# Optimization experiments

Measured on AMD Instinct MI355X. Metric: run time of the kernel, lower is better.

Reference implementation:

```python
import jax, jax.numpy as jnp
import numpy as np

B, C, H, W = 1, 256, 96, 96
C8 = C // 8
N = H * W


def setup_inputs() -> dict:
    key = jax.random.key(0)
    ks = jax.random.split(key, 12)
    inp = {
        "x": jax.random.normal(ks[0], (B, C, H, W), jnp.float32),
        "x_encoder": jax.random.normal(ks[1], (B, C, H, W), jnp.float32),
        # 1x1 conv params (weight stored as [out, in] matrices)
        "q_w": jax.random.normal(ks[2], (C8, C), jnp.float32) * 0.05,
        "q_b": jax.random.normal(ks[3], (C8,), jnp.float32) * 0.05,
        "k_w": jax.random.normal(ks[4], (C8, C), jnp.float32) * 0.05,
        "k_b": jax.random.normal(ks[5], (C8,), jnp.float32) * 0.05,
        "v_w": jax.random.normal(ks[6], (C, C), jnp.float32) * 0.05,
        "v_b": jax.random.normal(ks[7], (C,), jnp.float32) * 0.05,
        # positional bias parameters
        "h_pos": jax.random.normal(ks[8], (1, C8, H, 1), jnp.float32),
        "w_pos": jax.random.normal(ks[9], (1, C8, 1, W), jnp.float32),
        # gamma is zero-init in the module; use a random scalar for a non-trivial test
        "gamma": jax.random.normal(ks[10], (1,), jnp.float32),
    }
    return inp


def reference(x, x_encoder, q_w, q_b, k_w, k_b, v_w, v_b, h_pos, w_pos, gamma):
    b, c, h, w = x.shape
    n = h * w
    c8 = q_w.shape[0]
    # 1x1 convs == per-pixel linear maps
    query = (jnp.einsum('bchw,oc->bohw', x, q_w) + q_b[None, :, None, None])
    query = query.reshape(b, c8, n).transpose(0, 2, 1)            # [B, N, C8]
    key = (jnp.einsum('bchw,oc->bohw', x_encoder, k_w) + k_b[None, :, None, None])
    key = key.reshape(b, c8, n)                                   # [B, C8, N]
    # positional bias: broadcast-add then flatten, same as (height+width).view
    pos = (h_pos + w_pos).reshape(1, c8, n)                       # [1, C8, N]
    # energy = Q K^T + Q pos  ==  Q (K + pos)
    energy = jnp.einsum('bnc,bcm->bnm', query, key + pos)         # [B, N, N]
    attention = jax.nn.softmax(energy, axis=-1)
    value = (jnp.einsum('bchw,oc->bohw', x_encoder, v_w) + v_b[None, :, None, None])
    value = value.reshape(b, c, n)                                # [B, C, N]
    out = jnp.einsum('bcm,bnm->bcn', value, attention)            # [B, C, N]
    out = out.reshape(b, c, w, h)  # matches torch .view(B, C, W, H)
    return gamma * out + x
```

## Files before the change

### kernel.cpp

```cpp
#include <hip/hip_runtime.h>
#include <hip/hip_bf16.h>

#define NN 9216
#define CC 256
#define LOG2E 1.4426950408889634f

typedef __attribute__((ext_vector_type(8))) short short8;
typedef __attribute__((ext_vector_type(16))) float floatx16;
typedef __attribute__((ext_vector_type(4))) float floatx4;
typedef __attribute__((ext_vector_type(4))) unsigned short ushortx4;

#if __has_builtin(__builtin_amdgcn_exp2f)
#define fexp2 __builtin_amdgcn_exp2f
#else
#define fexp2 exp2f
#endif

__device__ __forceinline__ unsigned short f2bf(float f) {
    unsigned u = __float_as_uint(f);
    u = u + 0x7fffu + ((u >> 16) & 1u);
    return (unsigned short)(u >> 16);
}
__device__ __forceinline__ float bf2f(unsigned short s) {
    return __uint_as_float(((unsigned)s) << 16);
}
__device__ __forceinline__ unsigned pack2bf(float a, float b) {
    union { __hip_bfloat162 h; unsigned u; } cv;
    cv.h = __float22bfloat162_rn(make_float2(a, b));
    return cv.u;
}
__device__ __forceinline__ floatx16 mfma_bf16(short8 a, short8 b, floatx16 c) {
    return __builtin_amdgcn_mfma_f32_32x32x16_bf16(a, b, c, 0, 0, 0);
}

__global__ __launch_bounds__(256) void prep(
    const float* __restrict__ x, const float* __restrict__ xe,
    short* __restrict__ XBhi, short* __restrict__ XBlo,
    short* __restrict__ EBhi, short* __restrict__ EBlo)
{
    int t = threadIdx.x;
    const float* in = blockIdx.y ? xe : x;
    short* Dhi = blockIdx.y ? EBhi : XBhi;
    short* Dlo = blockIdx.y ? EBlo : XBlo;
    int tl = t & 31, sub = t >> 5;
    int nt = blockIdx.x >> 2, q4 = blockIdx.x & 3;
    int sub2 = q4 * 8 + sub;
    int kb_ = sub2 >> 1, hl = sub2 & 1;
    int n = nt * 32 + tl;
    int c0 = kb_ * 16 + hl * 8;
    union { unsigned short us[8]; short8 v8; } hi, lo;
#pragma unroll
    for (int j = 0; j < 8; ++j) {
        float val = in[(size_t)(c0 + j) * NN + n];
        unsigned short hb = f2bf(val);
        hi.us[j] = hb;
        lo.us[j] = f2bf(val - bf2f(hb));
    }
    size_t off = (((size_t)nt * 16 + kb_) * 64 + hl * 32 + tl) * 8;
    *(short8*)(Dhi + off) = hi.v8;
    *(short8*)(Dlo + off) = lo.v8;
}

__global__ __launch_bounds__(256) void wprep(
    const float* __restrict__ qw, const float* __restrict__ kw,
    const float* __restrict__ vw,
    short* __restrict__ WAhi, short* __restrict__ WAlo)
{
    int g = blockIdx.x * 256 + threadIdx.x;
    int lane = g & 63, kb_ = (g >> 6) & 15, ot = g >> 10;
    int o = lane & 31, half = lane >> 5;
    int c0 = kb_ * 16 + half * 8;
    const float* wsrc;
    int orow;
    float scale = 1.f;
    if (ot == 0) { wsrc = qw; orow = o; scale = LOG2E; }
    else if (ot == 1) { wsrc = kw; orow = o; }
    else { wsrc = vw; orow = (ot - 2) * 32 + o; }
    union { unsigned short us[8]; short8 v8; } hi, lo;
#pragma unroll
    for (int j = 0; j < 8; ++j) {
        float val = wsrc[(size_t)orow * 256 + c0 + j] * scale;
        unsigned short hb = f2bf(val);
        hi.us[j] = hb;
        lo.us[j] = f2bf(val - bf2f(hb));
    }
    size_t off = (((size_t)ot * 16 + kb_) * 64 + lane) * 8;
    *(short8*)(WAhi + off) = hi.v8;
    *(short8*)(WAlo + off) = lo.v8;
}

__global__ __launch_bounds__(256) void gemm_all(
    const short* __restrict__ XBhi, const short* __restrict__ XBlo,
    const short* __restrict__ EBhi, const short* __restrict__ EBlo,
    const short* __restrict__ WAhi, const short* __restrict__ WAlo,
    const float* __restrict__ qb, const float* __restrict__ kb,
    const float* __restrict__ hpos, const float* __restrict__ wpos,
    const float* __restrict__ vb,
    short* __restrict__ Qhi, short* __restrict__ Qlo,
    short* __restrict__ KP2, short* __restrict__ VF)
{
    __shared__ float lds[4][1024];
    int t = threadIdx.x;
    int wv = t >> 6, lane = t & 63, ln = lane & 31, h = lane >> 5;
    int nt = blockIdx.x * 2 + (wv & 1);
    int tile = blockIdx.y * 2 + (wv >> 1);

    const short* Bhi = (tile == 0 ? XBhi : EBhi) + (size_t)nt * 8192 + lane * 8;
    const short* Blo = (tile == 0 ? XBlo : EBlo) + (size_t)nt * 8192 + lane * 8;
    const short* Ahi = WAhi + (size_t)tile * 8192 + lane * 8;
    const short* Alo = WAlo + (size_t)tile * 8192 + lane * 8;

    floatx16 D;
#pragma unroll
    for (int r = 0; r < 16; ++r) D[r] = 0.f;
#pragma unroll
    for (int k = 0; k < 16; ++k) {
        short8 bh = *(const short8*)(Bhi + k * 512);
        short8 bl = *(const short8*)(Blo + k * 512);
        short8 ah = *(const short8*)(Ahi + k * 512);
        short8 al = *(const short8*)(Alo + k * 512);
        D = mfma_bf16(ah, bh, D);
        D = mfma_bf16(ah, bl, D);
        D = mfma_bf16(al, bh, D);
    }

    float* L = lds[wv];
#pragma unroll
    for (int r = 0; r < 16; ++r) {
        int row = (r & 3) + 8 * (r >> 2) + 4 * h;
        L[row * 32 + ((ln + row) & 31)] = D[r];
    }
    __syncthreads();

    if (tile == 0) {
        int n = nt * 32 + ln;
#pragma unroll
        for (int it = 0; it < 2; ++it) {
            int j0 = it * 16 + h * 8;
            union { unsigned short us[8]; short8 v8; } qh_, ql_;
#pragma unroll
            for (int jj = 0; jj < 8; ++jj) {
                int row = j0 + jj;
                float d = L[row * 32 + ((ln + row) & 31)] + qb[row] * LOG2E;
                unsigned short hb = f2bf(d);
                qh_.us[jj] = hb;
                ql_.us[jj] = f2bf(d - bf2f(hb));
            }
            *(short8*)(Qhi + (size_t)n * 32 + j0) = qh_.v8;
            *(short8*)(Qlo + (size_t)n * 32 + j0) = ql_.v8;
        }
    } else if (tile == 1) {
        int n = nt * 32 + ln;
        int hh = ((n >> 5) * 683) >> 11;
        int ww = n - hh * 96;
#pragma unroll
        for (int it = 0; it < 2; ++it) {
            int jb0 = it * 16 + h * 8;
            union { unsigned short us[8]; short8 v8; } o;
#pragma unroll
            for (int jj = 0; jj < 8; ++jj) {
                int row = jb0 + jj;
                float d = L[row * 32 + ((ln + row) & 31)]
                        + kb[row] + hpos[row * 96 + hh] + wpos[row * 96 + ww];
                o.us[jj] = f2bf(d);
            }
            *(short8*)(KP2 + (size_t)nt * 1024 + it * 512 + h * 256 + ln * 8) = o.v8;
        }
    } else {
        int cc = tile - 2;
        float bias = vb[cc * 32 + ln];
#pragma unroll
        for (int it = 0; it < 2; ++it) {
            union { unsigned short us[8]; short8 v8; } o;
#pragma unroll
            for (int ee = 0; ee < 8; ++ee) {
                int ml = it * 16 + h * 8 + ee;
                float d = L[ln * 32 + ((ml + ln) & 31)];
                o.us[ee] = f2bf(d + bias);
            }
            *(short8*)(VF + ((size_t)(nt * 2 + it) * 8 + cc) * 512 + lane * 8) = o.v8;
        }
    }
}

#define FSTEP(AH0, AH1, M0) do {                                                      \
    const size_t mo_ = (size_t)(M0) * 256;                                            \
    short8 va0 = *(const short8*)(Vb + mo_);                                          \
    short8 va1 = *(const short8*)(Vb + mo_ + 512);                                    \
    short8 va2 = *(const short8*)(Vb + mo_ + 1024);                                   \
    short8 va3 = *(const short8*)(Vb + mo_ + 1536);                                   \
    floatx16 S = {0.f,0.f,0.f,0.f,0.f,0.f,0.f,0.f,0.f,0.f,0.f,0.f,0.f,0.f,0.f,0.f};  \
    S = mfma_bf16(AH0, qf00, S);                                                      \
    S = mfma_bf16(AH0, qf01, S);                                                      \
    S = mfma_bf16(AH1, qf10, S);                                                      \
    S = mfma_bf16(AH1, qf11, S);                                                      \
    short8 va4 = *(const short8*)(Vb + mo_ + 2048);                                   \
    short8 va5 = *(const short8*)(Vb + mo_ + 2560);                                   \
    short8 va6 = *(const short8*)(Vb + mo_ + 3072);                                   \
    short8 va7 = *(const short8*)(Vb + mo_ + 3584);                                   \
    float ps = 0.f;                                                                   \
    _Pragma("unroll") for (int r = 0; r < 16; ++r) { S[r] = fexp2(S[r]); ps += S[r]; } \
    ps += __shfl_xor(ps, 32); l_run += ps;                                            \
    unsigned w0 = pack2bf(S[0], S[1]),  w1 = pack2bf(S[2], S[3]);                     \
    unsigned w2 = pack2bf(S[4], S[5]),  w3 = pack2bf(S[6], S[7]);                     \
    unsigned w4 = pack2bf(S[8], S[9]),  w5 = pack2bf(S[10], S[11]);                   \
    unsigned w6 = pack2bf(S[12], S[13]), w7 = pack2bf(S[14], S[15]);                  \
    {   unsigned p0 = h ? w0 : w2, p1 = h ? w1 : w3;                                  \
        unsigned e0 = (unsigned)__shfl_xor((int)p0, 32);                              \
        unsigned e1 = (unsigned)__shfl_xor((int)p1, 32);                              \
        union { unsigned u[4]; short8 v; } pf;                                        \
        pf.u[0] = h ? e0 : w0; pf.u[1] = h ? e1 : w1;                                 \
        pf.u[2] = h ? w2 : e0; pf.u[3] = h ? w3 : e1;                                 \
        O0 = mfma_bf16(va0, pf.v, O0); O1 = mfma_bf16(va1, pf.v, O1);                 \
        O2 = mfma_bf16(va2, pf.v, O2); O3 = mfma_bf16(va3, pf.v, O3);                 \
        O4 = mfma_bf16(va4, pf.v, O4); O5 = mfma_bf16(va5, pf.v, O5);                 \
        O6 = mfma_bf16(va6, pf.v, O6); O7 = mfma_bf16(va7, pf.v, O7); }               \
    short8 vb0 = *(const short8*)(Vb + mo_ + 4096);                                   \
    short8 vb1 = *(const short8*)(Vb + mo_ + 4608);                                   \
    short8 vb2 = *(const short8*)(Vb + mo_ + 5120);                                   \
    short8 vb3 = *(const short8*)(Vb + mo_ + 5632);                                   \
    short8 vb4 = *(const short8*)(Vb + mo_ + 6144);                                   \
    short8 vb5 = *(const short8*)(Vb + mo_ + 6656);                                   \
    short8 vb6 = *(const short8*)(Vb + mo_ + 7168);                                   \
    short8 vb7 = *(const short8*)(Vb + mo_ + 7680);                                   \
    {   unsigned p0 = h ? w4 : w6, p1 = h ? w5 : w7;                                  \
        unsigned e0 = (unsigned)__shfl_xor((int)p0, 32);                              \
        unsigned e1 = (unsigned)__shfl_xor((int)p1, 32);                              \
        union { unsigned u[4]; short8 v; } pf;                                        \
        pf.u[0] = h ? e0 : w4; pf.u[1] = h ? e1 : w5;                                 \
        pf.u[2] = h ? w6 : e0; pf.u[3] = h ? w7 : e1;                                 \
        O0 = mfma_bf16(vb0, pf.v, O0); O1 = mfma_bf16(vb1, pf.v, O1);                 \
        O2 = mfma_bf16(vb2, pf.v, O2); O3 = mfma_bf16(vb3, pf.v, O3);                 \
        O4 = mfma_bf16(vb4, pf.v, O4); O5 = mfma_bf16(vb5, pf.v, O5);                 \
        O6 = mfma_bf16(vb6, pf.v, O6); O7 = mfma_bf16(vb7, pf.v, O7); }               \
} while (0)

#define OGW(G, OG) { _Pragma("unroll") for (int r = 0; r < 16; ++r) { \
    int row = 32*(G) + (r & 3) + 8*(r >> 2) + 4*h;                    \
    Opart[obase + (size_t)row * NN + n0 + ln] = f2bf(OG[r]); } }

__global__ __launch_bounds__(128, 2) void flash(
    const short* __restrict__ Qhi, const short* __restrict__ Qlo,
    const short* __restrict__ KP2, const short* __restrict__ VT2,
    unsigned short* __restrict__ Opart, float* __restrict__ Lpart)
{
    int t = threadIdx.x;
    int wv = t >> 6;
    int lane = t & 63;
    int ln = lane & 31;
    int h = lane >> 5;
    int nt = blockIdx.x >> 2, mq = blockIdx.x & 3;
    int n0 = nt * 64 + wv * 32;
    int mstart = mq * 2304;

    int qoff = (n0 + ln) * 32 + h * 8;
    short8 qf00 = *(const short8*)(Qhi + qoff);
    short8 qf10 = *(const short8*)(Qhi + qoff + 16);
    short8 qf01 = *(const short8*)(Qlo + qoff);
    short8 qf11 = *(const short8*)(Qlo + qoff + 16);

    const short* Vb  = VT2 + (size_t)mstart * 256 + (size_t)lane * 8;
    const short* KPb = KP2 + (size_t)mstart * 32 + (size_t)lane * 8;

    floatx16 O0, O1, O2, O3, O4, O5, O6, O7;
#pragma unroll
    for (int r = 0; r < 16; ++r) {
        O0[r] = 0.f; O1[r] = 0.f; O2[r] = 0.f; O3[r] = 0.f;
        O4[r] = 0.f; O5[r] = 0.f; O6[r] = 0.f; O7[r] = 0.f;
    }
    float l_run = 0.f;

    short8 ahA0 = *(const short8*)(KPb);
    short8 ahA1 = *(const short8*)(KPb + 512);
    short8 ahB0, ahB1;

    for (int sp = 0; sp < 36; ++sp) {
        int m0 = sp * 64;
        ahB0 = *(const short8*)(KPb + (size_t)(m0 + 32) * 32);
        ahB1 = *(const short8*)(KPb + (size_t)(m0 + 32) * 32 + 512);
        FSTEP(ahA0, ahA1, m0);
        int nm = (sp < 35) ? (m0 + 64) : 0;
        ahA0 = *(const short8*)(KPb + (size_t)nm * 32);
        ahA1 = *(const short8*)(KPb + (size_t)nm * 32 + 512);
        FSTEP(ahB0, ahB1, m0 + 32);
    }

    if (lane < 32) Lpart[mq * NN + n0 + ln] = l_run;
    size_t obase = (size_t)mq * ((size_t)CC * NN);
    OGW(0,O0) OGW(1,O1) OGW(2,O2) OGW(3,O3) OGW(4,O4) OGW(5,O5) OGW(6,O6) OGW(7,O7)
}

__global__ __launch_bounds__(256) void stats(
    const float* __restrict__ Lpart, const float* __restrict__ gamma,
    float* __restrict__ W)
{
    int n = blockIdx.x * 256 + threadIdx.x;
    float L = Lpart[n] + Lpart[NN + n] + Lpart[2 * NN + n] + Lpart[3 * NN + n];
    W[n] = gamma[0] / L;
}

__global__ __launch_bounds__(256) void combine(
    const unsigned short* __restrict__ Opart, const float* __restrict__ W,
    const float* __restrict__ x, float* __restrict__ out)
{
    int i = blockIdx.x * 256 + threadIdx.x;
    int flat = i * 4;
    int n = flat % NN;
    floatx4 acc = *(const floatx4*)&x[flat];
    floatx4 w = *(const floatx4*)&W[n];
    float s0 = 0.f, s1 = 0.f, s2 = 0.f, s3 = 0.f;
#pragma unroll
    for (int q = 0; q < 4; ++q) {
        ushortx4 o = *(const ushortx4*)(Opart + (size_t)q * ((size_t)CC * NN) + flat);
        s0 += bf2f(o[0]); s1 += bf2f(o[1]); s2 += bf2f(o[2]); s3 += bf2f(o[3]);
    }
    acc[0] += s0 * w[0]; acc[1] += s1 * w[1]; acc[2] += s2 * w[2]; acc[3] += s3 * w[3];
    *(floatx4*)&out[flat] = acc;
}

extern "C" void kernel_launch(void* const* d_in, const int* in_sizes, int n_in,
                              void* d_out, int out_size, void* d_ws, size_t ws_size,
                              hipStream_t stream) {
    const float* x  = (const float*)d_in[0];
    const float* xe = (const float*)d_in[1];
    const float* qw = (const float*)d_in[2];
    const float* qb = (const float*)d_in[3];
    const float* kw = (const float*)d_in[4];
    const float* kb = (const float*)d_in[5];
    const float* vw = (const float*)d_in[6];
    const float* vb = (const float*)d_in[7];
    const float* hp = (const float*)d_in[8];
    const float* wp = (const float*)d_in[9];
    const float* gm = (const float*)d_in[10];

    char* ws = (char*)d_ws;
    short* Qhi  = (short*)(ws + 0);
    short* Qlo  = (short*)(ws + 589824);
    short* KP2  = (short*)(ws + 1179648);
    short* WAhi = (short*)(ws + 1769472);
    short* WAlo = (short*)(ws + 1933312);
    short* VF   = (short*)(ws + 2097152);
    unsigned short* Opart = (unsigned short*)(ws + 6815744);
    short* XBhi = (short*)(ws + 6815744);
    short* XBlo = (short*)(ws + 11534336);
    short* EBhi = (short*)(ws + 16252928);
    short* EBlo = (short*)(ws + 20971520);
    float* Lpart = (float*)(ws + 25837568);
    float* W     = (float*)(ws + 25985024);

    prep<<<dim3(1152, 2), dim3(256), 0, stream>>>(x, xe, XBhi, XBlo, EBhi, EBlo);
    wprep<<<dim3(40), dim3(256), 0, stream>>>(qw, kw, vw, WAhi, WAlo);
    gemm_all<<<dim3(144, 5), dim3(256), 0, stream>>>(
        XBhi, XBlo, EBhi, EBlo, WAhi, WAlo, qb, kb, hp, wp, vb, Qhi, Qlo, KP2, VF);
    flash<<<dim3(576), dim3(128), 0, stream>>>(Qhi, Qlo, KP2, VF, Opart, Lpart);
    stats<<<dim3(36), dim3(256), 0, stream>>>(Lpart, gm, W);
    combine<<<dim3(2304), dim3(256), 0, stream>>>(Opart, W, x, (float*)d_out);
}
```

Before: 112.2 us.

## Split output channels across blocks and reuse V fragments for two query tiles

```diff
diff --git a/kernel.cpp b/kernel.cpp
--- a/kernel.cpp
+++ b/kernel.cpp
@@ -183,24 +183,10 @@
     }
 }
 
-#define FSTEP(AH0, AH1, M0) do {                                                      \
-    const size_t mo_ = (size_t)(M0) * 256;                                            \
-    short8 va0 = *(const short8*)(Vb + mo_);                                          \
-    short8 va1 = *(const short8*)(Vb + mo_ + 512);                                    \
-    short8 va2 = *(const short8*)(Vb + mo_ + 1024);                                   \
-    short8 va3 = *(const short8*)(Vb + mo_ + 1536);                                   \
-    floatx16 S = {0.f,0.f,0.f,0.f,0.f,0.f,0.f,0.f,0.f,0.f,0.f,0.f,0.f,0.f,0.f,0.f};  \
-    S = mfma_bf16(AH0, qf00, S);                                                      \
-    S = mfma_bf16(AH0, qf01, S);                                                      \
-    S = mfma_bf16(AH1, qf10, S);                                                      \
-    S = mfma_bf16(AH1, qf11, S);                                                      \
-    short8 va4 = *(const short8*)(Vb + mo_ + 2048);                                   \
-    short8 va5 = *(const short8*)(Vb + mo_ + 2560);                                   \
-    short8 va6 = *(const short8*)(Vb + mo_ + 3072);                                   \
-    short8 va7 = *(const short8*)(Vb + mo_ + 3584);                                   \
+#define SMPV(S, V0, V1, V2, V3, U0, U1, U2, U3, OA, OB, OC, OD, LACC) do {            \
     float ps = 0.f;                                                                   \
     _Pragma("unroll") for (int r = 0; r < 16; ++r) { S[r] = fexp2(S[r]); ps += S[r]; } \
-    ps += __shfl_xor(ps, 32); l_run += ps;                                            \
+    ps += __shfl_xor(ps, 32); LACC += ps;                                             \
     unsigned w0 = pack2bf(S[0], S[1]),  w1 = pack2bf(S[2], S[3]);                     \
     unsigned w2 = pack2bf(S[4], S[5]),  w3 = pack2bf(S[6], S[7]);                     \
     unsigned w4 = pack2bf(S[8], S[9]),  w5 = pack2bf(S[10], S[11]);                   \
@@ -211,37 +197,25 @@
         union { unsigned u[4]; short8 v; } pf;                                        \
         pf.u[0] = h ? e0 : w0; pf.u[1] = h ? e1 : w1;                                 \
         pf.u[2] = h ? w2 : e0; pf.u[3] = h ? w3 : e1;                                 \
-        O0 = mfma_bf16(va0, pf.v, O0); O1 = mfma_bf16(va1, pf.v, O1);                 \
-        O2 = mfma_bf16(va2, pf.v, O2); O3 = mfma_bf16(va3, pf.v, O3);                 \
-        O4 = mfma_bf16(va4, pf.v, O4); O5 = mfma_bf16(va5, pf.v, O5);                 \
-        O6 = mfma_bf16(va6, pf.v, O6); O7 = mfma_bf16(va7, pf.v, O7); }               \
-    short8 vb0 = *(const short8*)(Vb + mo_ + 4096);                                   \
-    short8 vb1 = *(const short8*)(Vb + mo_ + 4608);                                   \
-    short8 vb2 = *(const short8*)(Vb + mo_ + 5120);                                   \
-    short8 vb3 = *(const short8*)(Vb + mo_ + 5632);                                   \
-    short8 vb4 = *(const short8*)(Vb + mo_ + 6144);                                   \
-    short8 vb5 = *(const short8*)(Vb + mo_ + 6656);                                   \
-    short8 vb6 = *(const short8*)(Vb + mo_ + 7168);                                   \
-    short8 vb7 = *(const short8*)(Vb + mo_ + 7680);                                   \
+        OA = mfma_bf16(V0, pf.v, OA); OB = mfma_bf16(V1, pf.v, OB);                   \
+        OC = mfma_bf16(V2, pf.v, OC); OD = mfma_bf16(V3, pf.v, OD); }                 \
     {   unsigned p0 = h ? w4 : w6, p1 = h ? w5 : w7;                                  \
         unsigned e0 = (unsigned)__shfl_xor((int)p0, 32);                              \
         unsigned e1 = (unsigned)__shfl_xor((int)p1, 32);                              \
         union { unsigned u[4]; short8 v; } pf;                                        \
         pf.u[0] = h ? e0 : w4; pf.u[1] = h ? e1 : w5;                                 \
         pf.u[2] = h ? w6 : e0; pf.u[3] = h ? w7 : e1;                                 \
-        O0 = mfma_bf16(vb0, pf.v, O0); O1 = mfma_bf16(vb1, pf.v, O1);                 \
-        O2 = mfma_bf16(vb2, pf.v, O2); O3 = mfma_bf16(vb3, pf.v, O3);                 \
-        O4 = mfma_bf16(vb4, pf.v, O4); O5 = mfma_bf16(vb5, pf.v, O5);                 \
-        O6 = mfma_bf16(vb6, pf.v, O6); O7 = mfma_bf16(vb7, pf.v, O7); }               \
+        OA = mfma_bf16(U0, pf.v, OA); OB = mfma_bf16(U1, pf.v, OB);                   \
+        OC = mfma_bf16(U2, pf.v, OC); OD = mfma_bf16(U3, pf.v, OD); }                 \
 } while (0)
 
-#define OGW(G, OG) { _Pragma("unroll") for (int r = 0; r < 16; ++r) { \
-    int row = 32*(G) + (r & 3) + 8*(r >> 2) + 4*h;                    \
-    Opart[obase + (size_t)row * NN + n0 + ln] = f2bf(OG[r]); } }
+#define OGW2(CF, T, OG) { _Pragma("unroll") for (int r = 0; r < 16; ++r) {            \
+    int row = ch * 128 + (CF) * 32 + (r & 3) + 8 * (r >> 2) + 4 * h;                  \
+    Opart[obase + (size_t)row * NN + n0 + (T) * 32 + ln] = f2bf(OG[r]); } }
 
 __global__ __launch_bounds__(128, 2) void flash(
     const short* __restrict__ Qhi, const short* __restrict__ Qlo,
-    const short* __restrict__ KP2, const short* __restrict__ VT2,
+    const short* __restrict__ KP2, const short* __restrict__ VF,
     unsigned short* __restrict__ Opart, float* __restrict__ Lpart)
 {
     int t = threadIdx.x;
@@ -249,45 +223,77 @@
     int lane = t & 63;
     int ln = lane & 31;
     int h = lane >> 5;
-    int nt = blockIdx.x >> 2, mq = blockIdx.x & 3;
-    int n0 = nt * 64 + wv * 32;
+    int bx = blockIdx.x;
+    int ntp = bx >> 3, mq = (bx >> 1) & 3, ch = bx & 1;
+    int n0 = ntp * 128 + wv * 64;
     int mstart = mq * 2304;
 
-    int qoff = (n0 + ln) * 32 + h * 8;
-    short8 qf00 = *(const short8*)(Qhi + qoff);
-    short8 qf10 = *(const short8*)(Qhi + qoff + 16);
-    short8 qf01 = *(const short8*)(Qlo + qoff);
-    short8 qf11 = *(const short8*)(Qlo + qoff + 16);
-
-    const short* Vb  = VT2 + (size_t)mstart * 256 + (size_t)lane * 8;
-    const short* KPb = KP2 + (size_t)mstart * 32 + (size_t)lane * 8;
-
-    floatx16 O0, O1, O2, O3, O4, O5, O6, O7;
+    int qoffA = (n0 + ln) * 32 + h * 8;
+    int qoffB = (n0 + 32 + ln) * 32 + h * 8;
+    short8 qAh0 = *(const short8*)(Qhi + qoffA);
+    short8 qAl0 = *(const short8*)(Qlo + qoffA);
+    short8 qAh1 = *(const short8*)(Qhi + qoffA + 16);
+    short8 qAl1 = *(const short8*)(Qlo + qoffA + 16);
+    short8 qBh0 = *(const short8*)(Qhi + qoffB);
+    short8 qBl0 = *(const short8*)(Qlo + qoffB);
+    short8 qBh1 = *(const short8*)(Qhi + qoffB + 16);
+    short8 qBl1 = *(const short8*)(Qlo + qoffB + 16);
+
+    const short* Vb  = VF + (size_t)(mstart >> 4) * 4096 + ch * 2048 + lane * 8;
+    const short* KPb = KP2 + (size_t)mstart * 32 + lane * 8;
+
+    floatx16 O00, O10, O20, O30, O01, O11, O21, O31;
 #pragma unroll
     for (int r = 0; r < 16; ++r) {
-        O0[r] = 0.f; O1[r] = 0.f; O2[r] = 0.f; O3[r] = 0.f;
-        O4[r] = 0.f; O5[r] = 0.f; O6[r] = 0.f; O7[r] = 0.f;
-    }
-    float l_run = 0.f;
-
-    short8 ahA0 = *(const short8*)(KPb);
-    short8 ahA1 = *(const short8*)(KPb + 512);
-    short8 ahB0, ahB1;
-
-    for (int sp = 0; sp < 36; ++sp) {
-        int m0 = sp * 64;
-        ahB0 = *(const short8*)(KPb + (size_t)(m0 + 32) * 32);
-        ahB1 = *(const short8*)(KPb + (size_t)(m0 + 32) * 32 + 512);
-        FSTEP(ahA0, ahA1, m0);
-        int nm = (sp < 35) ? (m0 + 64) : 0;
-        ahA0 = *(const short8*)(KPb + (size_t)nm * 32);
-        ahA1 = *(const short8*)(KPb + (size_t)nm * 32 + 512);
-        FSTEP(ahB0, ahB1, m0 + 32);
-    }
-
-    if (lane < 32) Lpart[mq * NN + n0 + ln] = l_run;
+        O00[r] = 0.f; O10[r] = 0.f; O20[r] = 0.f; O30[r] = 0.f;
+        O01[r] = 0.f; O11[r] = 0.f; O21[r] = 0.f; O31[r] = 0.f;
+    }
+    float l0 = 0.f, l1 = 0.f;
+
+    short8 ah0 = *(const short8*)(KPb);
+    short8 ah1 = *(const short8*)(KPb + 512);
+
+    for (int sp = 0; sp < 72; ++sp) {
+        const short* Vp = Vb + (size_t)sp * 8192;
+        short8 vf00 = *(const short8*)(Vp);
+        short8 vf10 = *(const short8*)(Vp + 512);
+        short8 vf20 = *(const short8*)(Vp + 1024);
+        short8 vf30 = *(const short8*)(Vp + 1536);
+        short8 vf01 = *(const short8*)(Vp + 4096);
+        short8 vf11 = *(const short8*)(Vp + 4608);
+        short8 vf21 = *(const short8*)(Vp + 5120);
+        short8 vf31 = *(const short8*)(Vp + 5632);
+
+        int nm = (sp < 71) ? sp + 1 : 0;
+        short8 an0 = *(const short8*)(KPb + (size_t)nm * 1024);
+        short8 an1 = *(const short8*)(KPb + (size_t)nm * 1024 + 512);
+
+        floatx16 SA = {0.f,0.f,0.f,0.f,0.f,0.f,0.f,0.f,0.f,0.f,0.f,0.f,0.f,0.f,0.f,0.f};
+        SA = mfma_bf16(ah0, qAh0, SA);
+        SA = mfma_bf16(ah0, qAl0, SA);
+        SA = mfma_bf16(ah1, qAh1, SA);
+        SA = mfma_bf16(ah1, qAl1, SA);
+        SMPV(SA, vf00, vf10, vf20, vf30, vf01, vf11, vf21, vf31,
+             O00, O10, O20, O30, l0);
+
+        floatx16 SB = {0.f,0.f,0.f,0.f,0.f,0.f,0.f,0.f,0.f,0.f,0.f,0.f,0.f,0.f,0.f,0.f};
+        SB = mfma_bf16(ah0, qBh0, SB);
+        SB = mfma_bf16(ah0, qBl0, SB);
+        SB = mfma_bf16(ah1, qBh1, SB);
+        SB = mfma_bf16(ah1, qBl1, SB);
+        SMPV(SB, vf00, vf10, vf20, vf30, vf01, vf11, vf21, vf31,
+             O01, O11, O21, O31, l1);
+
+        ah0 = an0; ah1 = an1;
+    }
+
+    if (ch == 0 && lane < 32) {
+        Lpart[mq * NN + n0 + ln] = l0;
+        Lpart[mq * NN + n0 + 32 + ln] = l1;
+    }
     size_t obase = (size_t)mq * ((size_t)CC * NN);
-    OGW(0,O0) OGW(1,O1) OGW(2,O2) OGW(3,O3) OGW(4,O4) OGW(5,O5) OGW(6,O6) OGW(7,O7)
+    OGW2(0, 0, O00) OGW2(1, 0, O10) OGW2(2, 0, O20) OGW2(3, 0, O30)
+    OGW2(0, 1, O01) OGW2(1, 1, O11) OGW2(2, 1, O21) OGW2(3, 1, O31)
 }
 
 __global__ __launch_bounds__(256) void stats(
```

Result: slower. 135.2 us (+20.5%).

## Split key range across waves in flash block and reduce partial outputs via LDS

Applied to the files above, without the earlier changes.

```diff
diff --git a/kernel.cpp b/kernel.cpp
--- a/kernel.cpp
+++ b/kernel.cpp
@@ -205,6 +205,7 @@
     unsigned w2 = pack2bf(S[4], S[5]),  w3 = pack2bf(S[6], S[7]);                     \
     unsigned w4 = pack2bf(S[8], S[9]),  w5 = pack2bf(S[10], S[11]);                   \
     unsigned w6 = pack2bf(S[12], S[13]), w7 = pack2bf(S[14], S[15]);                  \
+    __builtin_amdgcn_s_setprio(1);                                                    \
     {   unsigned p0 = h ? w0 : w2, p1 = h ? w1 : w3;                                  \
         unsigned e0 = (unsigned)__shfl_xor((int)p0, 32);                              \
         unsigned e1 = (unsigned)__shfl_xor((int)p1, 32);                              \
@@ -233,34 +234,44 @@
         O2 = mfma_bf16(vb2, pf.v, O2); O3 = mfma_bf16(vb3, pf.v, O3);                 \
         O4 = mfma_bf16(vb4, pf.v, O4); O5 = mfma_bf16(vb5, pf.v, O5);                 \
         O6 = mfma_bf16(vb6, pf.v, O6); O7 = mfma_bf16(vb7, pf.v, O7); }               \
+    __builtin_amdgcn_s_setprio(0);                                                    \
 } while (0)
 
-#define OGW(G, OG) { _Pragma("unroll") for (int r = 0; r < 16; ++r) { \
-    int row = 32*(G) + (r & 3) + 8*(r >> 2) + 4*h;                    \
-    Opart[obase + (size_t)row * NN + n0 + ln] = f2bf(OG[r]); } }
+#define OSHW(SL, OG) { _Pragma("unroll") for (int r = 0; r < 16; ++r) \
+    Osh[((SL) * 16 + r) * 64 + lane] = OG[r]; }
+#define OSTORE(G, OG) { _Pragma("unroll") for (int r = 0; r < 16; ++r) {   \
+    float v_ = OG[r] + Osh[((G) * 16 + r) * 64 + lane];                    \
+    int row = (G) * 32 + (r & 3) + 8 * (r >> 2) + 4 * h;                   \
+    Opart[obase + (size_t)row * NN + n0 + ln] = f2bf(v_); } }
 
 __global__ __launch_bounds__(128, 2) void flash(
     const short* __restrict__ Qhi, const short* __restrict__ Qlo,
-    const short* __restrict__ KP2, const short* __restrict__ VT2,
+    const short* __restrict__ KP2, const short* __restrict__ VF,
     unsigned short* __restrict__ Opart, float* __restrict__ Lpart)
 {
+    __shared__ float Osh[8192];
+    __shared__ float Lsh[2][32];
+
     int t = threadIdx.x;
     int wv = t >> 6;
     int lane = t & 63;
     int ln = lane & 31;
     int h = lane >> 5;
-    int nt = blockIdx.x >> 2, mq = blockIdx.x & 3;
-    int n0 = nt * 64 + wv * 32;
-    int mstart = mq * 2304;
+    int g = blockIdx.x;
+    int xc = g & 7;
+    int mq = xc >> 1;
+    int nt = (g >> 3) * 2 + (xc & 1);
+    int n0 = nt * 32;
+    int mw = mq * 2304 + wv * 1152;
 
     int qoff = (n0 + ln) * 32 + h * 8;
     short8 qf00 = *(const short8*)(Qhi + qoff);
+    short8 qf01 = *(const short8*)(Qlo + qoff);
     short8 qf10 = *(const short8*)(Qhi + qoff + 16);
-    short8 qf01 = *(const short8*)(Qlo + qoff);
     short8 qf11 = *(const short8*)(Qlo + qoff + 16);
 
-    const short* Vb  = VT2 + (size_t)mstart * 256 + (size_t)lane * 8;
-    const short* KPb = KP2 + (size_t)mstart * 32 + (size_t)lane * 8;
+    const short* Vb  = VF + (size_t)mw * 256 + (size_t)lane * 8;
+    const short* KPb = KP2 + (size_t)mw * 32 + (size_t)lane * 8;
 
     floatx16 O0, O1, O2, O3, O4, O5, O6, O7;
 #pragma unroll
@@ -274,20 +285,28 @@
     short8 ahA1 = *(const short8*)(KPb + 512);
     short8 ahB0, ahB1;
 
-    for (int sp = 0; sp < 36; ++sp) {
+    for (int sp = 0; sp < 18; ++sp) {
         int m0 = sp * 64;
         ahB0 = *(const short8*)(KPb + (size_t)(m0 + 32) * 32);
         ahB1 = *(const short8*)(KPb + (size_t)(m0 + 32) * 32 + 512);
         FSTEP(ahA0, ahA1, m0);
-        int nm = (sp < 35) ? (m0 + 64) : 0;
+        int nm = (sp < 17) ? (m0 + 64) : 0;
         ahA0 = *(const short8*)(KPb + (size_t)nm * 32);
         ahA1 = *(const short8*)(KPb + (size_t)nm * 32 + 512);
         FSTEP(ahB0, ahB1, m0 + 32);
     }
 
-    if (lane < 32) Lpart[mq * NN + n0 + ln] = l_run;
+    if (lane < 32) Lsh[wv][ln] = l_run;
+    if (wv == 1) { OSHW(0, O0) OSHW(1, O1) OSHW(2, O2) OSHW(3, O3) }
+    else         { OSHW(4, O4) OSHW(5, O5) OSHW(6, O6) OSHW(7, O7) }
+    __syncthreads();
     size_t obase = (size_t)mq * ((size_t)CC * NN);
-    OGW(0,O0) OGW(1,O1) OGW(2,O2) OGW(3,O3) OGW(4,O4) OGW(5,O5) OGW(6,O6) OGW(7,O7)
+    if (wv == 0) {
+        OSTORE(0, O0) OSTORE(1, O1) OSTORE(2, O2) OSTORE(3, O3)
+        if (lane < 32) Lpart[mq * NN + n0 + ln] = Lsh[0][ln] + Lsh[1][ln];
+    } else {
+        OSTORE(4, O4) OSTORE(5, O5) OSTORE(6, O6) OSTORE(7, O7)
+    }
 }
 
 __global__ __launch_bounds__(256) void stats(
@@ -352,7 +371,7 @@
     wprep<<<dim3(40), dim3(256), 0, stream>>>(qw, kw, vw, WAhi, WAlo);
     gemm_all<<<dim3(144, 5), dim3(256), 0, stream>>>(
         XBhi, XBlo, EBhi, EBlo, WAhi, WAlo, qb, kb, hp, wp, vb, Qhi, Qlo, KP2, VF);
-    flash<<<dim3(576), dim3(128), 0, stream>>>(Qhi, Qlo, KP2, VF, Opart, Lpart);
+    flash<<<dim3(1152), dim3(128), 0, stream>>>(Qhi, Qlo, KP2, VF, Opart, Lpart);
     stats<<<dim3(36), dim3(256), 0, stream>>>(Lpart, gm, W);
     combine<<<dim3(2304), dim3(256), 0, stream>>>(Opart, W, x, (float*)d_out);
 }
```

After: 137.8 us. 22.8% more time.

## Double-buffer V fragments across flash steps and fold stats into combine

Applied to the files above, without the earlier changes.

```diff
diff --git a/kernel.cpp b/kernel.cpp
--- a/kernel.cpp
+++ b/kernel.cpp
@@ -183,21 +183,33 @@
     }
 }
 
-#define FSTEP(AH0, AH1, M0) do {                                                      \
-    const size_t mo_ = (size_t)(M0) * 256;                                            \
-    short8 va0 = *(const short8*)(Vb + mo_);                                          \
-    short8 va1 = *(const short8*)(Vb + mo_ + 512);                                    \
-    short8 va2 = *(const short8*)(Vb + mo_ + 1024);                                   \
-    short8 va3 = *(const short8*)(Vb + mo_ + 1536);                                   \
+#define PFV(VN, MOFF) do {                                                            \
+    const short* Vp_ = Vb + (size_t)(MOFF) * 256;                                     \
+    VN##0  = *(const short8*)(Vp_);                                                   \
+    VN##1  = *(const short8*)(Vp_ + 512);                                             \
+    VN##2  = *(const short8*)(Vp_ + 1024);                                            \
+    VN##3  = *(const short8*)(Vp_ + 1536);                                            \
+    VN##4  = *(const short8*)(Vp_ + 2048);                                            \
+    VN##5  = *(const short8*)(Vp_ + 2560);                                            \
+    VN##6  = *(const short8*)(Vp_ + 3072);                                            \
+    VN##7  = *(const short8*)(Vp_ + 3584);                                            \
+    VN##8  = *(const short8*)(Vp_ + 4096);                                            \
+    VN##9  = *(const short8*)(Vp_ + 4608);                                            \
+    VN##10 = *(const short8*)(Vp_ + 5120);                                            \
+    VN##11 = *(const short8*)(Vp_ + 5632);                                            \
+    VN##12 = *(const short8*)(Vp_ + 6144);                                            \
+    VN##13 = *(const short8*)(Vp_ + 6656);                                            \
+    VN##14 = *(const short8*)(Vp_ + 7168);                                            \
+    VN##15 = *(const short8*)(Vp_ + 7680);                                            \
+} while (0)
+
+#define FSTEPP(AH0, AH1, VC, VN, MNEXT) do {                                          \
+    PFV(VN, MNEXT);                                                                   \
     floatx16 S = {0.f,0.f,0.f,0.f,0.f,0.f,0.f,0.f,0.f,0.f,0.f,0.f,0.f,0.f,0.f,0.f};  \
     S = mfma_bf16(AH0, qf00, S);                                                      \
     S = mfma_bf16(AH0, qf01, S);                                                      \
     S = mfma_bf16(AH1, qf10, S);                                                      \
     S = mfma_bf16(AH1, qf11, S);                                                      \
-    short8 va4 = *(const short8*)(Vb + mo_ + 2048);                                   \
-    short8 va5 = *(const short8*)(Vb + mo_ + 2560);                                   \
-    short8 va6 = *(const short8*)(Vb + mo_ + 3072);                                   \
-    short8 va7 = *(const short8*)(Vb + mo_ + 3584);                                   \
     float ps = 0.f;                                                                   \
     _Pragma("unroll") for (int r = 0; r < 16; ++r) { S[r] = fexp2(S[r]); ps += S[r]; } \
     ps += __shfl_xor(ps, 32); l_run += ps;                                            \
@@ -211,35 +223,27 @@
         union { unsigned u[4]; short8 v; } pf;                                        \
         pf.u[0] = h ? e0 : w0; pf.u[1] = h ? e1 : w1;                                 \
         pf.u[2] = h ? w2 : e0; pf.u[3] = h ? w3 : e1;                                 \
-        O0 = mfma_bf16(va0, pf.v, O0); O1 = mfma_bf16(va1, pf.v, O1);                 \
-        O2 = mfma_bf16(va2, pf.v, O2); O3 = mfma_bf16(va3, pf.v, O3);                 \
-        O4 = mfma_bf16(va4, pf.v, O4); O5 = mfma_bf16(va5, pf.v, O5);                 \
-        O6 = mfma_bf16(va6, pf.v, O6); O7 = mfma_bf16(va7, pf.v, O7); }               \
-    short8 vb0 = *(const short8*)(Vb + mo_ + 4096);                                   \
-    short8 vb1 = *(const short8*)(Vb + mo_ + 4608);                                   \
-    short8 vb2 = *(const short8*)(Vb + mo_ + 5120);                                   \
-    short8 vb3 = *(const short8*)(Vb + mo_ + 5632);                                   \
-    short8 vb4 = *(const short8*)(Vb + mo_ + 6144);                                   \
-    short8 vb5 = *(const short8*)(Vb + mo_ + 6656);                                   \
-    short8 vb6 = *(const short8*)(Vb + mo_ + 7168);                                   \
-    short8 vb7 = *(const short8*)(Vb + mo_ + 7680);                                   \
+        O0 = mfma_bf16(VC##0, pf.v, O0); O1 = mfma_bf16(VC##1, pf.v, O1);             \
+        O2 = mfma_bf16(VC##2, pf.v, O2); O3 = mfma_bf16(VC##3, pf.v, O3);             \
+        O4 = mfma_bf16(VC##4, pf.v, O4); O5 = mfma_bf16(VC##5, pf.v, O5);             \
+        O6 = mfma_bf16(VC##6, pf.v, O6); O7 = mfma_bf16(VC##7, pf.v, O7); }           \
     {   unsigned p0 = h ? w4 : w6, p1 = h ? w5 : w7;                                  \
         unsigned e0 = (unsigned)__shfl_xor((int)p0, 32);                              \
         unsigned e1 = (unsigned)__shfl_xor((int)p1, 32);                              \
         union { unsigned u[4]; short8 v; } pf;                                        \
         pf.u[0] = h ? e0 : w4; pf.u[1] = h ? e1 : w5;                                 \
         pf.u[2] = h ? w6 : e0; pf.u[3] = h ? w7 : e1;                                 \
-        O0 = mfma_bf16(vb0, pf.v, O0); O1 = mfma_bf16(vb1, pf.v, O1);                 \
-        O2 = mfma_bf16(vb2, pf.v, O2); O3 = mfma_bf16(vb3, pf.v, O3);                 \
-        O4 = mfma_bf16(vb4, pf.v, O4); O5 = mfma_bf16(vb5, pf.v, O5);                 \
-        O6 = mfma_bf16(vb6, pf.v, O6); O7 = mfma_bf16(vb7, pf.v, O7); }               \
+        O0 = mfma_bf16(VC##8,  pf.v, O0); O1 = mfma_bf16(VC##9,  pf.v, O1);           \
+        O2 = mfma_bf16(VC##10, pf.v, O2); O3 = mfma_bf16(VC##11, pf.v, O3);           \
+        O4 = mfma_bf16(VC##12, pf.v, O4); O5 = mfma_bf16(VC##13, pf.v, O5);           \
+        O6 = mfma_bf16(VC##14, pf.v, O6); O7 = mfma_bf16(VC##15, pf.v, O7); }         \
 } while (0)
 
 #define OGW(G, OG) { _Pragma("unroll") for (int r = 0; r < 16; ++r) { \
-    int row = 32*(G) + (r & 3) + 8*(r >> 2) + 4*h;                    \
+    int row = 32*(G) + (r & 3) + 8 * (r >> 2) + 4 * h;                \
     Opart[obase + (size_t)row * NN + n0 + ln] = f2bf(OG[r]); } }
 
-__global__ __launch_bounds__(128, 2) void flash(
+__global__ __launch_bounds__(128) void flash(
     const short* __restrict__ Qhi, const short* __restrict__ Qlo,
     const short* __restrict__ KP2, const short* __restrict__ VT2,
     unsigned short* __restrict__ Opart, float* __restrict__ Lpart)
@@ -270,6 +274,12 @@
     }
     float l_run = 0.f;
 
+    short8 vA0, vA1, vA2, vA3, vA4, vA5, vA6, vA7;
+    short8 vA8, vA9, vA10, vA11, vA12, vA13, vA14, vA15;
+    short8 vB0, vB1, vB2, vB3, vB4, vB5, vB6, vB7;
+    short8 vB8, vB9, vB10, vB11, vB12, vB13, vB14, vB15;
+
+    PFV(vA, 0);
     short8 ahA0 = *(const short8*)(KPb);
     short8 ahA1 = *(const short8*)(KPb + 512);
     short8 ahB0, ahB1;
@@ -278,43 +288,43 @@
         int m0 = sp * 64;
         ahB0 = *(const short8*)(KPb + (size_t)(m0 + 32) * 32);
         ahB1 = *(const short8*)(KPb + (size_t)(m0 + 32) * 32 + 512);
-        FSTEP(ahA0, ahA1, m0);
+        FSTEPP(ahA0, ahA1, vA, vB, m0 + 32);
         int nm = (sp < 35) ? (m0 + 64) : 0;
         ahA0 = *(const short8*)(KPb + (size_t)nm * 32);
         ahA1 = *(const short8*)(KPb + (size_t)nm * 32 + 512);
-        FSTEP(ahB0, ahB1, m0 + 32);
+        FSTEPP(ahB0, ahB1, vB, vA, nm);
     }
 
     if (lane < 32) Lpart[mq * NN + n0 + ln] = l_run;
     size_t obase = (size_t)mq * ((size_t)CC * NN);
-    OGW(0,O0) OGW(1,O1) OGW(2,O2) OGW(3,O3) OGW(4,O4) OGW(5,O5) OGW(6,O6) OGW(7,O7)
-}
-
-__global__ __launch_bounds__(256) void stats(
-    const float* __restrict__ Lpart, const float* __restrict__ gamma,
-    float* __restrict__ W)
-{
-    int n = blockIdx.x * 256 + threadIdx.x;
-    float L = Lpart[n] + Lpart[NN + n] + Lpart[2 * NN + n] + Lpart[3 * NN + n];
-    W[n] = gamma[0] / L;
+    OGW(0, O0) OGW(1, O1) OGW(2, O2) OGW(3, O3)
+    OGW(4, O4) OGW(5, O5) OGW(6, O6) OGW(7, O7)
 }
 
 __global__ __launch_bounds__(256) void combine(
-    const unsigned short* __restrict__ Opart, const float* __restrict__ W,
-    const float* __restrict__ x, float* __restrict__ out)
+    const unsigned short* __restrict__ Opart, const float* __restrict__ Lpart,
+    const float* __restrict__ gamma, const float* __restrict__ x,
+    float* __restrict__ out)
 {
     int i = blockIdx.x * 256 + threadIdx.x;
     int flat = i * 4;
     int n = flat % NN;
     floatx4 acc = *(const floatx4*)&x[flat];
-    floatx4 w = *(const floatx4*)&W[n];
+    floatx4 L0 = *(const floatx4*)&Lpart[n];
+    floatx4 L1 = *(const floatx4*)&Lpart[NN + n];
+    floatx4 L2 = *(const floatx4*)&Lpart[2 * NN + n];
+    floatx4 L3 = *(const floatx4*)&Lpart[3 * NN + n];
+    float g = gamma[0];
     float s0 = 0.f, s1 = 0.f, s2 = 0.f, s3 = 0.f;
 #pragma unroll
     for (int q = 0; q < 4; ++q) {
         ushortx4 o = *(const ushortx4*)(Opart + (size_t)q * ((size_t)CC * NN) + flat);
         s0 += bf2f(o[0]); s1 += bf2f(o[1]); s2 += bf2f(o[2]); s3 += bf2f(o[3]);
     }
-    acc[0] += s0 * w[0]; acc[1] += s1 * w[1]; acc[2] += s2 * w[2]; acc[3] += s3 * w[3];
+    acc[0] += s0 * (g / (L0[0] + L1[0] + L2[0] + L3[0]));
+    acc[1] += s1 * (g / (L0[1] + L1[1] + L2[1] + L3[1]));
+    acc[2] += s2 * (g / (L0[2] + L1[2] + L2[2] + L3[2]));
+    acc[3] += s3 * (g / (L0[3] + L1[3] + L2[3] + L3[3]));
     *(floatx4*)&out[flat] = acc;
 }
 
@@ -346,13 +356,11 @@
     short* EBhi = (short*)(ws + 16252928);
     short* EBlo = (short*)(ws + 20971520);
     float* Lpart = (float*)(ws + 25837568);
-    float* W     = (float*)(ws + 25985024);
 
     prep<<<dim3(1152, 2), dim3(256), 0, stream>>>(x, xe, XBhi, XBlo, EBhi, EBlo);
     wprep<<<dim3(40), dim3(256), 0, stream>>>(qw, kw, vw, WAhi, WAlo);
     gemm_all<<<dim3(144, 5), dim3(256), 0, stream>>>(
         XBhi, XBlo, EBhi, EBlo, WAhi, WAlo, qb, kb, hp, wp, vb, Qhi, Qlo, KP2, VF);
     flash<<<dim3(576), dim3(128), 0, stream>>>(Qhi, Qlo, KP2, VF, Opart, Lpart);
-    stats<<<dim3(36), dim3(256), 0, stream>>>(Lpart, gm, W);
-    combine<<<dim3(2304), dim3(256), 0, stream>>>(Opart, W, x, (float*)d_out);
-}
+    combine<<<dim3(2304), dim3(256), 0, stream>>>(Opart, Lpart, gm, x, (float*)d_out);
+}
```

Measured after the change: 135.7 us. 1.21x slower.
